# Kernel optimization log

Measured on AMD Instinct MI355X. Metric: run time of the kernel, lower is better.

The kernel has to match this reference:

```python
import jax, jax.numpy as jnp
import numpy as np

DIM = 1024
KV_DIM = 1024
WINDOW_SIZE = 64  # band half-width = 32, band width W = 65
B, S = 2, 2048


def setup_inputs() -> dict:
    key = jax.random.key(0)
    ks = jax.random.split(key, 12)
    w_scale = 1.0 / np.sqrt(DIM)
    return {
        "x": jax.random.normal(ks[0], (B, S, DIM), dtype=jnp.float32),
        # neural_memory: Linear(dim, kv) -> ReLU -> Linear(kv, dim); weights stored [in, out]
        "nm_w1": jax.random.normal(ks[1], (DIM, KV_DIM), dtype=jnp.float32) * w_scale,
        "nm_b1": jnp.zeros((KV_DIM,), dtype=jnp.float32),
        "nm_w2": jax.random.normal(ks[2], (KV_DIM, DIM), dtype=jnp.float32) * w_scale,
        "nm_b2": jnp.zeros((DIM,), dtype=jnp.float32),
        # SlidingWindowAttention projections (dim -> dim)
        "q_w": jax.random.normal(ks[3], (DIM, DIM), dtype=jnp.float32) * w_scale,
        "q_b": jnp.zeros((DIM,), dtype=jnp.float32),
        "k_w": jax.random.normal(ks[4], (DIM, DIM), dtype=jnp.float32) * w_scale,
        "k_b": jnp.zeros((DIM,), dtype=jnp.float32),
        "v_w": jax.random.normal(ks[5], (DIM, DIM), dtype=jnp.float32) * w_scale,
        "v_b": jnp.zeros((DIM,), dtype=jnp.float32),
    }


def _sliding_window_attention(m, q_w, q_b, k_w, k_b, v_w, v_b, window_size):
    # m: [B, S, D]. Per position i, attend to [i - w//2, i + w//2] inclusive.
    Bsz, Seq, D = m.shape
    q = m @ q_w + q_b
    k = m @ k_w + k_b
    v = m @ v_w + v_b
    half = window_size // 2
    offsets = jnp.arange(-half, half + 1)                # [W]
    idx = jnp.arange(Seq)[:, None] + offsets[None, :]    # [S, W]
    valid = (idx >= 0) & (idx < Seq)                     # [S, W]
    idx_c = jnp.clip(idx, 0, Seq - 1)
    k_band = k[:, idx_c]                                 # [B, S, W, D]
    v_band = v[:, idx_c]                                 # [B, S, W, D]
    scale = 1.0 / jnp.sqrt(jnp.float32(D))
    scores = jnp.einsum("bsd,bswd->bsw", q, k_band) * scale
    scores = jnp.where(valid[None, :, :], scores, -jnp.inf)
    weights = jax.nn.softmax(scores, axis=-1)            # [B, S, W]
    return jnp.einsum("bsw,bswd->bsd", weights, v_band)


def reference(x, nm_w1, nm_b1, nm_w2, nm_b2, q_w, q_b, k_w, k_b, v_w, v_b):
    # Faithful output path of LongTermMemory.forward: the key/value-proj MSE
    # surprise update mutates key_proj weights in-place (no_grad) but does NOT
    # affect the returned tensor o, which is swa(neural_memory(x)).
    h = jax.nn.relu(x @ nm_w1 + nm_b1)
    m = h @ nm_w2 + nm_b2                                # neural_memory(x): [B, S, D]
    return _sliding_window_attention(m, q_w, q_b, k_w, k_b, v_w, v_b, WINDOW_SIZE)
```

## Files before the change

kernel.cpp:

```cpp
#include <hip/hip_runtime.h>
#include <cstdint>

#define DIMN 1024
#define SEQ  2048
#define BATCH 2
#define MTOT (BATCH*SEQ)
#define NELEM_ACT (MTOT*DIMN)
#define NELEM_W   (DIMN*DIMN)

typedef __attribute__((ext_vector_type(8))) short   s16x8;
typedef __attribute__((ext_vector_type(4))) float   f32x4v;

__device__ __forceinline__ float b2f(unsigned short u) {
  union { unsigned int i; float f; } x; x.i = ((unsigned int)u) << 16; return x.f;
}
__device__ __forceinline__ unsigned short f2b(float f) {
  unsigned int x = __float_as_uint(f);
  return (unsigned short)((x + 0x7fffu + ((x >> 16) & 1u)) >> 16);
}

__device__ __forceinline__ void gload16(const void* g, void* l) {
  __builtin_amdgcn_global_load_lds((const __attribute__((address_space(1))) void*)g,
                                   (__attribute__((address_space(3))) void*)l,
                                   16, 0, 0);
}

__global__ __launch_bounds__(256) void cvt_kernel(
    const float* __restrict__ in, unsigned short* __restrict__ out, int n) {
  int i = (blockIdx.x * 256 + threadIdx.x) * 8;
  if (i >= n) return;
  float4 v0 = *(const float4*)(in + i);
  float4 v1 = *(const float4*)(in + i + 4);
  ushort4 a, b;
  a.x = f2b(v0.x); a.y = f2b(v0.y); a.z = f2b(v0.z); a.w = f2b(v0.w);
  b.x = f2b(v1.x); b.y = f2b(v1.y); b.z = f2b(v1.z); b.w = f2b(v1.w);
  *(ushort4*)(out + i) = a;
  *(ushort4*)(out + i + 4) = b;
}

__global__ __launch_bounds__(256) void transpose5_kernel(
    const float* __restrict__ w1, const float* __restrict__ w2,
    const float* __restrict__ qw, const float* __restrict__ kw,
    const float* __restrict__ vw,
    unsigned short* __restrict__ w1t, unsigned short* __restrict__ w2t,
    unsigned short* __restrict__ wqkvt) {
  __shared__ float t[32][33];
  int z = blockIdx.z;
  const float* in = (z == 0) ? w1 : (z == 1) ? w2 : (z == 2) ? qw : (z == 3) ? kw : vw;
  unsigned short* dst = (z == 0) ? w1t : (z == 1) ? w2t : wqkvt + (size_t)(z - 2) * NELEM_W;

  int tx = threadIdx.x & 31, ty = threadIdx.x >> 5;
  int r0 = blockIdx.y * 32, c0 = blockIdx.x * 32;
  #pragma unroll
  for (int i = 0; i < 32; i += 8)
    t[ty + i][tx] = in[(size_t)(r0 + ty + i) * DIMN + c0 + tx];
  __syncthreads();
  #pragma unroll
  for (int i = 0; i < 32; i += 8)
    dst[(size_t)(c0 + ty + i) * DIMN + r0 + tx] = f2b(t[tx][ty + i]);
}

template<int MF, int NF, int EPI>
__global__ __launch_bounds__(256) void gemm_kernel(
    const unsigned short* __restrict__ A, const unsigned short* __restrict__ Bt,
    const float* __restrict__ bias0, const float* __restrict__ bias1,
    const float* __restrict__ bias2,
    unsigned short* __restrict__ O, unsigned short* __restrict__ O2,
    int Ndim, int Kdim) {
  constexpr int TB = (MF + NF) * 4;
  __shared__ unsigned short lds[2 * TB * 512];

  const int tid  = threadIdx.x;
  const int lane = tid & 63;
  const int wave = tid >> 6;
  const int wm = wave >> 1;
  const int wn = wave & 1;
  const int frow = lane & 15;
  const int krow = lane >> 4;
  const int bm0 = blockIdx.y * (MF * 32);
  const int bn0 = blockIdx.x * (NF * 32);

  f32x4v acc[MF][NF] = {};

  auto stage = [&](unsigned short* dst, int k0) {
    #pragma unroll
    for (int t = 0; t < TB / 4; ++t) {
      int i = wave + t * 4;
      const unsigned short* src;
      if (i < MF * 4) {
        int mf = i >> 1, ds = i & 1;
        src = A + (size_t)(bm0 + mf * 16 + frow) * Kdim + k0 + ds * 32 + krow * 8;
      } else {
        int j = i - MF * 4;
        int nf = j >> 1, ds = j & 1;
        src = Bt + (size_t)(bn0 + nf * 16 + frow) * Kdim + k0 + ds * 32 + krow * 8;
      }
      gload16(src, dst + i * 512);
    }
  };

  auto compute = [&](const unsigned short* buf) {
    const short* sl = (const short*)buf;
    #pragma unroll
    for (int ds = 0; ds < 2; ++ds) {
      s16x8 a[MF], b[NF];
      #pragma unroll
      for (int m = 0; m < MF; ++m)
        a[m] = *(const s16x8*)(sl + ((wm * MF + m) * 2 + ds) * 512 + lane * 8);
      #pragma unroll
      for (int n = 0; n < NF; ++n)
        b[n] = *(const s16x8*)(sl + (MF * 4 + (wn * NF + n) * 2 + ds) * 512 + lane * 8);
      #pragma unroll
      for (int m = 0; m < MF; ++m)
        #pragma unroll
        for (int n = 0; n < NF; ++n)
          acc[m][n] = __builtin_amdgcn_mfma_f32_16x16x32_bf16(a[m], b[n], acc[m][n], 0, 0, 0);
    }
  };

  const int nt = Kdim >> 6;
  stage(lds, 0);
  for (int t = 0; t < nt; t += 2) {
    __syncthreads();
    if (t + 1 < nt) stage(lds + TB * 512, (t + 1) << 6);
    compute(lds);
    __syncthreads();
    if (t + 2 < nt) stage(lds, (t + 2) << 6);
    compute(lds + TB * 512);
  }

  #pragma unroll
  for (int n = 0; n < NF; ++n) {
    int col = bn0 + wn * (NF * 16) + n * 16 + frow;
    float bv;
    if (EPI == 2) {
      int sel = col >> 10;
      const float* bp = (sel == 0) ? bias0 : (sel == 1) ? bias1 : bias2;
      bv = bp[col & (DIMN - 1)];
    } else {
      bv = bias0[col];
    }
    #pragma unroll
    for (int m = 0; m < MF; ++m) {
      int rbase = bm0 + wm * (MF * 16) + m * 16 + krow * 4;
      if (EPI == 2 && col >= 2048) {
        int d = col - 2048;
        ushort4 pk;
        pk.x = f2b(acc[m][n][0] + bv); pk.y = f2b(acc[m][n][1] + bv);
        pk.z = f2b(acc[m][n][2] + bv); pk.w = f2b(acc[m][n][3] + bv);
        *(ushort4*)(O2 + (size_t)d * MTOT + rbase) = pk;
      } else {
        #pragma unroll
        for (int r = 0; r < 4; ++r) {
          float v = acc[m][n][r] + bv;
          if (EPI == 0) v = fmaxf(v, 0.f);
          if (EPI == 2) O[(size_t)(rbase + r) * 2048 + col] = f2b(v);
          else          O[(size_t)(rbase + r) * Ndim + col] = f2b(v);
        }
      }
    }
  }
}

#define QBLK 32
#define NEGI (-1.0e30f)

__global__ __launch_bounds__(256) void attn_mfma_kernel(
    const unsigned short* __restrict__ qk,
    const unsigned short* __restrict__ vt,
    float* __restrict__ out) {
  __shared__ unsigned short stage[24 * 512];
  __shared__ unsigned short plds[QBLK][136];
  __shared__ float pmax[2][QBLK];
  __shared__ float psum[2][QBLK];

  const int tid = threadIdx.x, lane = tid & 63, wave = tid >> 6;
  const int frow = lane & 15, krow = lane >> 4;
  const int tok0 = blockIdx.x * QBLK;
  const int s0 = tok0 & (SEQ - 1);
  const int bbase = tok0 - s0;
  const int qf = wave & 1;
  const int kh = wave >> 1;

  f32x4v sacc[3] = {};
  for (int d0 = 0; d0 < DIMN; d0 += 64) {
    #pragma unroll
    for (int t = 0; t < 4; ++t) {
      int i = wave + t * 4;
      const unsigned short* src;
      if (i < 4) {
        int qfs = i >> 1, ds = i & 1;
        src = qk + (size_t)(tok0 + qfs * 16 + frow) * 2048 + d0 + ds * 32 + krow * 8;
      } else {
        int j = i - 4;
        int kf = j >> 1, ds = j & 1;
        int kpos = s0 - 32 + kf * 16 + frow;
        kpos = min(max(kpos, 0), SEQ - 1);
        src = qk + (size_t)(bbase + kpos) * 2048 + 1024 + d0 + ds * 32 + krow * 8;
      }
      gload16(src, stage + i * 512);
    }
    __syncthreads();
    const short* sl = (const short*)stage;
    #pragma unroll
    for (int ds = 0; ds < 2; ++ds) {
      s16x8 bq = *(const s16x8*)(sl + (qf * 2 + ds) * 512 + lane * 8);
      #pragma unroll
      for (int f = 0; f < 3; ++f) {
        int kf = kh * 3 + f;
        s16x8 ak = *(const s16x8*)(sl + (4 + kf * 2 + ds) * 512 + lane * 8);
        sacc[f] = __builtin_amdgcn_mfma_f32_16x16x32_bf16(ak, bq, sacc[f], 0, 0, 0);
      }
    }
    __syncthreads();
  }

  const int qloc = qf * 16 + frow;
  const int qpos = s0 + qloc;
  float sv[3][4];
  float mx = NEGI;
  #pragma unroll
  for (int f = 0; f < 3; ++f) {
    #pragma unroll
    for (int r = 0; r < 4; ++r) {
      int kloc = (kh * 3 + f) * 16 + krow * 4 + r;
      int kpos = s0 - 32 + kloc;
      int dd = kpos - qpos;
      bool valid = (dd >= -32) && (dd <= 32) && (kpos >= 0) && (kpos < SEQ);
      float v = valid ? sacc[f][r] * 0.03125f : NEGI;
      sv[f][r] = v;
      mx = fmaxf(mx, v);
    }
  }
  mx = fmaxf(mx, __shfl_xor(mx, 16));
  mx = fmaxf(mx, __shfl_xor(mx, 32));
  if (lane < 16) pmax[kh][qf * 16 + lane] = mx;
  __syncthreads();
  float M = fmaxf(pmax[0][qloc], pmax[1][qloc]);
  float sum = 0.f;
  unsigned int pw[3][2];
  #pragma unroll
  for (int f = 0; f < 3; ++f) {
    #pragma unroll
    for (int pr = 0; pr < 2; ++pr) {
      float p0 = __expf(sv[f][2 * pr]     - M);
      float p1 = __expf(sv[f][2 * pr + 1] - M);
      sum += p0 + p1;
      pw[f][pr] = (unsigned int)f2b(p0) | ((unsigned int)f2b(p1) << 16);
    }
  }
  sum += __shfl_xor(sum, 16);
  sum += __shfl_xor(sum, 32);
  if (lane < 16) psum[kh][qf * 16 + lane] = sum;
  {
    unsigned int* pl = (unsigned int*)&plds[0][0];
    int base = qloc * 68 + (kh * 3) * 8 + krow * 2;
    #pragma unroll
    for (int f = 0; f < 3; ++f) {
      pl[base + f * 8 + 0] = pw[f][0];
      pl[base + f * 8 + 1] = pw[f][1];
    }
  }
  __syncthreads();

  s16x8 pa[3];
  #pragma unroll
  for (int kf = 0; kf < 3; ++kf)
    pa[kf] = *(const s16x8*)((const short*)&plds[0][0] +
                             (qf * 16 + frow) * 136 + kf * 32 + krow * 8);
  float rden[4];
  #pragma unroll
  for (int r = 0; r < 4; ++r) {
    int q = qf * 16 + krow * 4 + r;
    rden[r] = 1.f / (psum[0][q] + psum[1][q]);
  }

  for (int c = 0; c < 8; ++c) {
    #pragma unroll
    for (int t = 0; t < 6; ++t) {
      int i = wave + t * 4;
      int kf = i >> 3, nf = i & 7;
      int d = c * 128 + nf * 16 + frow;
      int tt = s0 - 32 + kf * 32 + krow * 8;
      tt = min(max(tt, 0), SEQ - 8);
      gload16(vt + (size_t)d * MTOT + bbase + tt, stage + i * 512);
    }
    __syncthreads();
    const short* sl = (const short*)stage;
    f32x4v oacc[4] = {};
    #pragma unroll
    for (int kf = 0; kf < 3; ++kf) {
      #pragma unroll
      for (int n = 0; n < 4; ++n) {
        int nf = kh * 4 + n;
        s16x8 bv = *(const s16x8*)(sl + (kf * 8 + nf) * 512 + lane * 8);
        oacc[n] = __builtin_amdgcn_mfma_f32_16x16x32_bf16(pa[kf], bv, oacc[n], 0, 0, 0);
      }
    }
    #pragma unroll
    for (int n = 0; n < 4; ++n) {
      int d = c * 128 + (kh * 4 + n) * 16 + frow;
      #pragma unroll
      for (int r = 0; r < 4; ++r) {
        int q = qf * 16 + krow * 4 + r;
        out[(size_t)(tok0 + q) * DIMN + d] = oacc[n][r] * rden[r];
      }
    }
    __syncthreads();
  }
}

extern "C" void kernel_launch(void* const* d_in, const int* in_sizes, int n_in,
                              void* d_out, int out_size, void* d_ws, size_t ws_size,
                              hipStream_t stream) {
  const float* x  = (const float*)d_in[0];
  const float* w1 = (const float*)d_in[1];
  const float* b1 = (const float*)d_in[2];
  const float* w2 = (const float*)d_in[3];
  const float* b2 = (const float*)d_in[4];
  const float* qw = (const float*)d_in[5];
  const float* qb = (const float*)d_in[6];
  const float* kw = (const float*)d_in[7];
  const float* kb = (const float*)d_in[8];
  const float* vw = (const float*)d_in[9];
  const float* vb = (const float*)d_in[10];
  float* out = (float*)d_out;

  char* ws = (char*)d_ws;
  const size_t MB = 1024 * 1024;
  unsigned short* x_bf  = (unsigned short*)(ws);
  unsigned short* h_bf  = (unsigned short*)(ws + 8  * MB);
  unsigned short* m_bf  = (unsigned short*)(ws + 16 * MB);
  unsigned short* qkbuf = (unsigned short*)(ws + 24 * MB);
  unsigned short* vtbuf = (unsigned short*)(ws + 40 * MB);
  unsigned short* w1t   = (unsigned short*)(ws + 48 * MB);
  unsigned short* w2t   = (unsigned short*)(ws + 50 * MB);
  unsigned short* wqkvt = (unsigned short*)(ws + 52 * MB);

  cvt_kernel<<<NELEM_ACT / (256 * 8), 256, 0, stream>>>(x, x_bf, NELEM_ACT);
  transpose5_kernel<<<dim3(32, 32, 5), 256, 0, stream>>>(w1, w2, qw, kw, vw,
                                                         w1t, w2t, wqkvt);

  dim3 g1(DIMN / 128, MTOT / 64);
  gemm_kernel<2, 4, 0><<<g1, 256, 0, stream>>>(x_bf, w1t, b1, nullptr, nullptr,
                                               h_bf, nullptr, DIMN, DIMN);
  gemm_kernel<2, 4, 1><<<g1, 256, 0, stream>>>(h_bf, w2t, b2, nullptr, nullptr,
                                               m_bf, nullptr, DIMN, DIMN);
  dim3 g2(3 * DIMN / 128, MTOT / 128);
  gemm_kernel<4, 4, 2><<<g2, 256, 0, stream>>>(m_bf, wqkvt, qb, kb, vb,
                                               qkbuf, vtbuf, 3 * DIMN, DIMN);

  attn_mfma_kernel<<<MTOT / QBLK, 256, 0, stream>>>(qkbuf, vtbuf, out);
}
```

Before: 234.0 us.

## Deepen GEMM prefetch with explicit vmcnt waits and remap tiles for L2 locality

Restructures the GEMM main loop so both LDS buffers are prefetched up front. Each compute step now waits only for its own stage's loads, using explicit s_waitcnt vmcnt counts instead of a full __syncthreads drain, so global-to-LDS loads for the next tile can overlap the current compute. It also remaps workgroup IDs with a stride-8 swizzle so neighbouring tiles are grouped differently, aiming at better cache reuse. The cost is reliance on exact vmcnt accounting per wave; an unlisted NL value trips the static_assert, and a miscount would race on LDS.

```diff
diff --git a/kernel.cpp b/kernel.cpp
--- a/kernel.cpp
+++ b/kernel.cpp
@@ -23,6 +23,13 @@
   __builtin_amdgcn_global_load_lds((const __attribute__((address_space(1))) void*)g,
                                    (__attribute__((address_space(3))) void*)l,
                                    16, 0, 0);
+}
+
+template<int N> __device__ __forceinline__ void waitvm() {
+  static_assert(N == 0 || N == 6 || N == 8, "add a case");
+  if constexpr (N == 0) asm volatile("s_waitcnt vmcnt(0)" ::: "memory");
+  else if constexpr (N == 6) asm volatile("s_waitcnt vmcnt(6)" ::: "memory");
+  else if constexpr (N == 8) asm volatile("s_waitcnt vmcnt(8)" ::: "memory");
 }
 
 __global__ __launch_bounds__(256) void cvt_kernel(
@@ -68,6 +75,7 @@
     unsigned short* __restrict__ O, unsigned short* __restrict__ O2,
     int Ndim, int Kdim) {
   constexpr int TB = (MF + NF) * 4;
+  constexpr int NL = TB / 4;
   __shared__ unsigned short lds[2 * TB * 512];
 
   const int tid  = threadIdx.x;
@@ -77,14 +85,20 @@
   const int wn = wave & 1;
   const int frow = lane & 15;
   const int krow = lane >> 4;
-  const int bm0 = blockIdx.y * (MF * 32);
-  const int bn0 = blockIdx.x * (NF * 32);
+
+  const int nwg = gridDim.x * gridDim.y;
+  const int orig = blockIdx.y * gridDim.x + blockIdx.x;
+  const int tile = (orig & 7) * (nwg >> 3) + (orig >> 3);
+  const int bx = tile % gridDim.x;
+  const int by = tile / gridDim.x;
+  const int bm0 = by * (MF * 32);
+  const int bn0 = bx * (NF * 32);
 
   f32x4v acc[MF][NF] = {};
 
   auto stage = [&](unsigned short* dst, int k0) {
     #pragma unroll
-    for (int t = 0; t < TB / 4; ++t) {
+    for (int t = 0; t < NL; ++t) {
       int i = wave + t * 4;
       const unsigned short* src;
       if (i < MF * 4) {
@@ -118,15 +132,27 @@
     }
   };
 
+  unsigned short* lds0 = lds;
+  unsigned short* lds1 = lds + TB * 512;
   const int nt = Kdim >> 6;
-  stage(lds, 0);
+
+  stage(lds0, 0);
+  stage(lds1, 64);
   for (int t = 0; t < nt; t += 2) {
-    __syncthreads();
-    if (t + 1 < nt) stage(lds + TB * 512, (t + 1) << 6);
-    compute(lds);
-    __syncthreads();
-    if (t + 2 < nt) stage(lds, (t + 2) << 6);
-    compute(lds + TB * 512);
+    bool pfA = (t + 2 < nt);
+    if (pfA) waitvm<NL>(); else waitvm<0>();
+    __builtin_amdgcn_s_barrier();
+    __builtin_amdgcn_sched_barrier(0);
+    compute(lds0);
+    __builtin_amdgcn_s_barrier();
+    if (pfA) stage(lds0, (t + 2) << 6);
+    bool pfB = (t + 3 < nt);
+    if (pfA) { if (pfB) waitvm<NL>(); else waitvm<0>(); } else waitvm<0>();
+    __builtin_amdgcn_s_barrier();
+    __builtin_amdgcn_sched_barrier(0);
+    compute(lds1);
+    __builtin_amdgcn_s_barrier();
+    if (pfB) stage(lds1, (t + 3) << 6);
   }
 
   #pragma unroll
```

After: 229.1 us. 2.1% less time.

## Use four-stage LDS pipeline with K=32 tiles and explicit vmcnt waits

Applied to the files above, without the earlier changes.

Replaces the double-buffered K=64 staging in the GEMM with a four-deep ring of K=32 stages. Each phase waits only on the oldest in-flight loads via explicit s_waitcnt vmcnt instead of a full __syncthreads drain. The aim is to keep more global-to-LDS loads in flight and hide memory latency behind MFMA work. The cost is smaller compute chunks per barrier, more barriers, and hand-managed wait counts that could be wrong if the compiler issues other vector memory ops.

```diff
diff --git a/kernel.cpp b/kernel.cpp
--- a/kernel.cpp
+++ b/kernel.cpp
@@ -23,6 +23,17 @@
   __builtin_amdgcn_global_load_lds((const __attribute__((address_space(1))) void*)g,
                                    (__attribute__((address_space(3))) void*)l,
                                    16, 0, 0);
+}
+
+template<int N> __device__ __forceinline__ void waitvm() {
+  if constexpr (N == 0)       asm volatile("s_waitcnt vmcnt(0)" ::: "memory");
+  else if constexpr (N == 3)  asm volatile("s_waitcnt vmcnt(3)" ::: "memory");
+  else if constexpr (N == 4)  asm volatile("s_waitcnt vmcnt(4)" ::: "memory");
+  else if constexpr (N == 6)  asm volatile("s_waitcnt vmcnt(6)" ::: "memory");
+  else if constexpr (N == 8)  asm volatile("s_waitcnt vmcnt(8)" ::: "memory");
+  else if constexpr (N == 9)  asm volatile("s_waitcnt vmcnt(9)" ::: "memory");
+  else if constexpr (N == 12) asm volatile("s_waitcnt vmcnt(12)" ::: "memory");
+  else static_assert(N == 0, "add a case");
 }
 
 __global__ __launch_bounds__(256) void cvt_kernel(
@@ -67,8 +78,9 @@
     const float* __restrict__ bias2,
     unsigned short* __restrict__ O, unsigned short* __restrict__ O2,
     int Ndim, int Kdim) {
-  constexpr int TB = (MF + NF) * 4;
-  __shared__ unsigned short lds[2 * TB * 512];
+  constexpr int TB = (MF + NF) * 2;
+  constexpr int NL = TB / 4;
+  __shared__ unsigned short lds[4 * TB * 512];
 
   const int tid  = threadIdx.x;
   const int lane = tid & 63;
@@ -84,16 +96,14 @@
 
   auto stage = [&](unsigned short* dst, int k0) {
     #pragma unroll
-    for (int t = 0; t < TB / 4; ++t) {
+    for (int t = 0; t < NL; ++t) {
       int i = wave + t * 4;
       const unsigned short* src;
-      if (i < MF * 4) {
-        int mf = i >> 1, ds = i & 1;
-        src = A + (size_t)(bm0 + mf * 16 + frow) * Kdim + k0 + ds * 32 + krow * 8;
+      if (i < MF * 2) {
+        src = A + (size_t)(bm0 + i * 16 + frow) * Kdim + k0 + krow * 8;
       } else {
-        int j = i - MF * 4;
-        int nf = j >> 1, ds = j & 1;
-        src = Bt + (size_t)(bn0 + nf * 16 + frow) * Kdim + k0 + ds * 32 + krow * 8;
+        int j = i - MF * 2;
+        src = Bt + (size_t)(bn0 + j * 16 + frow) * Kdim + k0 + krow * 8;
       }
       gload16(src, dst + i * 512);
     }
@@ -101,32 +111,48 @@
 
   auto compute = [&](const unsigned short* buf) {
     const short* sl = (const short*)buf;
-    #pragma unroll
-    for (int ds = 0; ds < 2; ++ds) {
-      s16x8 a[MF], b[NF];
-      #pragma unroll
-      for (int m = 0; m < MF; ++m)
-        a[m] = *(const s16x8*)(sl + ((wm * MF + m) * 2 + ds) * 512 + lane * 8);
+    s16x8 a[MF], b[NF];
+    #pragma unroll
+    for (int m = 0; m < MF; ++m)
+      a[m] = *(const s16x8*)(sl + (wm * MF + m) * 512 + lane * 8);
+    #pragma unroll
+    for (int n = 0; n < NF; ++n)
+      b[n] = *(const s16x8*)(sl + (MF * 2 + wn * NF + n) * 512 + lane * 8);
+    #pragma unroll
+    for (int m = 0; m < MF; ++m)
       #pragma unroll
       for (int n = 0; n < NF; ++n)
-        b[n] = *(const s16x8*)(sl + (MF * 4 + (wn * NF + n) * 2 + ds) * 512 + lane * 8);
-      #pragma unroll
-      for (int m = 0; m < MF; ++m)
-        #pragma unroll
-        for (int n = 0; n < NF; ++n)
-          acc[m][n] = __builtin_amdgcn_mfma_f32_16x16x32_bf16(a[m], b[n], acc[m][n], 0, 0, 0);
-    }
+        acc[m][n] = __builtin_amdgcn_mfma_f32_16x16x32_bf16(a[m], b[n], acc[m][n], 0, 0, 0);
   };
 
-  const int nt = Kdim >> 6;
-  stage(lds, 0);
-  for (int t = 0; t < nt; t += 2) {
-    __syncthreads();
-    if (t + 1 < nt) stage(lds + TB * 512, (t + 1) << 6);
-    compute(lds);
-    __syncthreads();
-    if (t + 2 < nt) stage(lds, (t + 2) << 6);
-    compute(lds + TB * 512);
+  const int nt = Kdim >> 5;
+  unsigned short* b0 = lds;
+  unsigned short* b1 = lds + TB * 512;
+  unsigned short* b2 = lds + 2 * TB * 512;
+  unsigned short* b3 = lds + 3 * TB * 512;
+
+  stage(b0, 0); stage(b1, 32); stage(b2, 64); stage(b3, 96);
+
+  for (int t = 0; t < nt; t += 4) {
+    #define PHASE(P, BUF)                                                     \
+    {                                                                         \
+      int s = t + P;                                                          \
+      int rem = nt - 1 - s;                                      \
+      if (rem >= 3)      waitvm<3 * NL>();                                    \
+      else if (rem == 2) waitvm<2 * NL>();                                    \
+      else if (rem == 1) waitvm<NL>();                                        \
+      else               waitvm<0>();                                         \
+      __builtin_amdgcn_s_barrier();                                           \
+      __builtin_amdgcn_sched_barrier(0);                                      \
+      compute(BUF);                                                           \
+      __builtin_amdgcn_s_barrier();                                           \
+      if (s + 4 < nt) stage(BUF, (s + 4) << 5);                               \
+    }
+    PHASE(0, b0)
+    PHASE(1, b1)
+    PHASE(2, b2)
+    PHASE(3, b3)
+    #undef PHASE
   }
 
   #pragma unroll
```

Result: faster. 228.7 us (-2.3%).
